# Kernel optimization log

Measured on AMD Instinct MI355X. Metric: run time of the kernel, lower is better.

The kernel has to match this reference:

```python
import jax, jax.numpy as jnp
import numpy as np
from jax import lax

SAMPLE_RATE = 44100.0  # config['std_sample_rate']
LOG9 = float(np.log(9.0))


def _drc_single(x, p):
    # param sanitization (apply_drc): NaN -> 0, 0 -> 1e-10, then rescale
    p = jnp.where(jnp.isnan(p), jnp.zeros_like(p), p)
    p = jnp.where(p == 0, jnp.full_like(p, 1e-10), p)
    threshold = -p[0] * 60.0
    ratio = p[1] * 10.0
    attack_time = jnp.maximum(p[2] / 10.0, 1e-4)
    release_time = jnp.maximum(p[3] * 3.0, 0.005)
    knee_dB = p[4] * 24.0
    makeup_gain_dB = p[5] * 20.0

    alpha_A = jnp.exp(-LOG9 / (SAMPLE_RATE * attack_time))
    alpha_R = jnp.exp(-LOG9 / (SAMPLE_RATE * release_time))

    # level detection in dB
    x_G = jnp.clip(20.0 * jnp.log10(jnp.abs(x) + 1e-8), -96.0, None)

    # static gain curve with soft knee (exactly as in source)
    below = 2.0 * (x_G - threshold) < -knee_dB
    above = 2.0 * (x_G - threshold) > knee_dB
    y_knee = x_G + (1.0 / ratio) * ((x_G - threshold + knee_dB) / 2.0) ** 2 / (2.0 * knee_dB)
    y_above = threshold + (x_G - threshold) / ratio
    y_G = jnp.where(below, x_G, jnp.where(above, y_above, y_knee))

    x_L = x_G - y_G  # gain reduction target (dB)

    # branching attack/release one-pole smoother; y_L[0] = 0, loop from n=1
    def step(y_prev, xl):
        alpha = jnp.where(xl > y_prev, alpha_A, alpha_R)
        y = alpha * y_prev + (1.0 - alpha) * xl
        return y, y

    _, y_tail = lax.scan(step, jnp.zeros((), x.dtype), x_L[1:])
    y_L = jnp.concatenate([jnp.zeros((1,), x.dtype), y_tail])
    y_L = jnp.clip(y_L, -96.0, None)

    y = x * jnp.power(10.0, -y_L / 20.0) * jnp.power(10.0, makeup_gain_dB / 20.0)
    # non-finite scrub (apply_drc tail)
    return jnp.where(jnp.isfinite(y), y, jnp.zeros_like(y))


def setup_inputs() -> dict:
    key = jax.random.key(0)
    kx, kp = jax.random.split(key)
    B, N = 16, 524288
    x = jax.random.normal(kx, (B, N), dtype=jnp.float32) * 0.3
    params = jax.random.uniform(kp, (B, 6), dtype=jnp.float32)
    return {"x": x, "params": params}


def reference(x, params):
    return jax.vmap(_drc_single)(x, params)
```

## Files before the change

### kernel.cpp

```cpp
#include <hip/hip_runtime.h>
#include <math.h>


#define SRATE 44100.0f
#define KSTEP 255
#define INTC  256
#define TILE2 32
#define NEG_INF -1e38f

static __device__ __forceinline__ float san(float p){
    p = isnan(p) ? 0.0f : p;
    p = (p == 0.0f) ? 1e-10f : p;
    return p;
}

struct Consts {
    float thr, invr, knee, i2k;
    float aA, aR, kAs, kRs, s;
    float mk;
    float LA, LR;
};

static __device__ __forceinline__ Consts get_consts(const float* __restrict__ P, int b){
    float p0 = san(P[b*6+0]);
    float p1 = san(P[b*6+1]);
    float p2 = san(P[b*6+2]);
    float p3 = san(P[b*6+3]);
    float p4 = san(P[b*6+4]);
    float p5 = san(P[b*6+5]);
    Consts c;
    c.thr  = -p0 * 60.0f;
    float ratio = p1 * 10.0f;
    c.invr = 1.0f / ratio;
    float atk = fmaxf(p2 / 10.0f, 1e-4f);
    float rel = fmaxf(p3 * 3.0f, 0.005f);
    c.knee = p4 * 24.0f;
    c.i2k  = 1.0f / (2.0f * c.knee);
    const float LOG9 = 2.1972245773362196f;
    const float INVLN2 = 1.4426950408889634f;
    c.aA = expf(-LOG9 / (SRATE * atk));
    c.aR = expf(-LOG9 / (SRATE * rel));
    c.LA = (-LOG9 / (SRATE * atk)) * INVLN2;
    c.LR = (-LOG9 / (SRATE * rel)) * INVLN2;
    c.s  = (c.aA <= c.aR) ? 1.0f : -1.0f;
    c.kAs = c.s * (1.0f - c.aA);
    c.kRs = c.s * (1.0f - c.aR);
    c.mk = exp2f((p5 * 20.0f) * 0.16609640474436813f);
    return c;
}

static __device__ __forceinline__ float compute_xl(float xin, const Consts& c){
    float ax = fabsf(xin) + 1e-8f;
    float xg = fmaxf(20.0f * log10f(ax), -96.0f);
    float d  = xg - c.thr;
    float t2 = d + d;
    float u  = (d + c.knee) * 0.5f;
    float yk = xg + (c.invr * (u * u)) * c.i2k;
    float ya = c.thr + d * c.invr;
    float yg = (t2 < -c.knee) ? xg : ((t2 > c.knee) ? ya : yk);
    return xg - yg;
}

template<int CTRL>
static __device__ __forceinline__ float maxdpp(float v){
    int t = __builtin_amdgcn_update_dpp(__float_as_int(v), __float_as_int(v),
                                        CTRL, 0xF, 0xF, false);
    return fmaxf(v, __int_as_float(t));
}

static __device__ __forceinline__ float rdlane(float v, int l){
    return __int_as_float(__builtin_amdgcn_readlane(__float_as_int(v), l));
}

#define STEPA(xli) { \
    float ca = c.kAs * (xli); \
    float cr = c.kRs * (xli); \
    float p3 = __shfl_up(M3, 1, 64); \
    p3 = (lane == 0) ? NEG_INF : p3; \
    M3 = fmaxf(fmaf(c.aA, M2, ca), fmaf(c.aR, M3, cr)); \
    M2 = fmaxf(fmaf(c.aA, M1, ca), fmaf(c.aR, M2, cr)); \
    M1 = fmaxf(fmaf(c.aA, M0, ca), fmaf(c.aR, M1, cr)); \
    M0 = fmaxf(fmaf(c.aA, p3, ca), fmaf(c.aR, M0, cr)); \
}

__global__ __launch_bounds__(256) void drc_passA(
    const float* __restrict__ x, const float* __restrict__ P,
    float* __restrict__ Mout, float* __restrict__ Movf,
    int N, int NBLK, int tailSteps, unsigned CAP4)
{
    const int lane = threadIdx.x & 63;
    const int gw = blockIdx.x * 4 + (threadIdx.x >> 6);
    const int batch = blockIdx.y;
    if (gw >= NBLK) return;
    Consts c = get_consts(P, batch);
    const int t = (gw == NBLK - 1) ? tailSteps : KSTEP;
    const size_t base = (size_t)batch * N;
    const int n0 = 2 + KSTEP * gw;

    const int i0 = n0 + 4 * lane;
    float xl0 = compute_xl(x[base + min(i0 + 0, N - 1)], c);
    float xl1 = compute_xl(x[base + min(i0 + 1, N - 1)], c);
    float xl2 = compute_xl(x[base + min(i0 + 2, N - 1)], c);
    float xl3 = compute_xl(x[base + min(i0 + 3, N - 1)], c);

    float M0 = (lane == 0) ? 0.0f : NEG_INF;
    float M1 = NEG_INF, M2 = NEG_INF, M3 = NEG_INF;

    if (t == KSTEP){
        for (int g = 0; g < 64; ++g){
            float xa0 = rdlane(xl0, g);
            float xa1 = rdlane(xl1, g);
            float xa2 = rdlane(xl2, g);
            float xa3 = rdlane(xl3, g);
            STEPA(xa0);
            STEPA(xa1);
            STEPA(xa2);
            if (g < 63) { STEPA(xa3); }
        }
    } else {
        for (int g = 0; g < 64; ++g){
            int ib = 4 * g;
            if (ib >= t) break;
            float xa0 = rdlane(xl0, g);
            float xa1 = rdlane(xl1, g);
            float xa2 = rdlane(xl2, g);
            float xa3 = rdlane(xl3, g);
            if (ib + 0 < t) { STEPA(xa0); }
            if (ib + 1 < t) { STEPA(xa1); }
            if (ib + 2 < t) { STEPA(xa2); }
            if (ib + 3 < t) { STEPA(xa3); }
        }
    }

    const size_t f4 = ((size_t)batch * NBLK + gw) * 64 + lane;
    float4 v = { M0, M1, M2, M3 };
    if (f4 < CAP4) ((float4*)Mout)[f4] = v;
    else           ((float4*)Movf)[f4 - CAP4] = v;
}

__global__ __launch_bounds__(192) void drc_chain(
    const float* __restrict__ x, const float* __restrict__ P,
    const float* __restrict__ Mout, const float* __restrict__ Movf,
    float* __restrict__ entries, int N, int NBLK, unsigned CAP4)
{
    const int batch = blockIdx.x;
    const int tid = threadIdx.x;
    const int lane = tid & 63;
    const int w = tid >> 6;
    Consts c = get_consts(P, batch);

    __shared__ float sM[2][TILE2 * INTC];

    const float4* outM4 = (const float4*)Mout;
    const float4* ovf4  = (const float4*)Movf;
    float* ent = entries + (size_t)batch * NBLK;

    const float j0 = (float)(4 * lane);
    float sl0 = exp2f((j0 + 0.0f) * c.LA + (float)(KSTEP - 4*lane - 0) * c.LR);
    float sl1 = exp2f((j0 + 1.0f) * c.LA + (float)(KSTEP - 4*lane - 1) * c.LR);
    float sl2 = exp2f((j0 + 2.0f) * c.LA + (float)(KSTEP - 4*lane - 2) * c.LR);
    float sl3 = exp2f((j0 + 3.0f) * c.LA + (float)(KSTEP - 4*lane - 3) * c.LR);

    float xl1 = compute_xl(x[(size_t)batch * N + 1], c);
    float z = fmaxf(c.kAs * xl1, c.kRs * xl1);

    const int NMAIN = NBLK - 1;
    const int ntiles = (NMAIN + TILE2 - 1) / TILE2;

    auto loadM4 = [&](size_t f4) -> float4 {
        return (f4 < CAP4) ? outM4[f4] : ovf4[f4 - CAP4];
    };

    auto stage = [&](int tile, int buf){
        const int s = tid - 64;
        const int b0 = tile * TILE2;
        const int cnt = min(TILE2, NMAIN - b0);
        const int total4 = cnt * 64;
        const size_t fb = ((size_t)batch * NBLK + b0) * 64;
        float4* dst = (float4*)&sM[buf][0];
        if (total4 == TILE2 * 64){
            float4 tmp[16];
            #pragma unroll
            for (int k = 0; k < 16; ++k) tmp[k] = loadM4(fb + (size_t)k * 128 + s);
            #pragma unroll
            for (int k = 0; k < 16; ++k) dst[k * 128 + s] = tmp[k];
        } else {
            for (int q = s; q < total4; q += 128) dst[q] = loadM4(fb + q);
        }
    };

    if (w > 0 && ntiles > 0) stage(0, 0);
    __syncthreads();

    float eacc = 0.0f;
    int ebase = 0;

    for (int tile = 0; tile < ntiles; ++tile){
        const int buf = tile & 1;
        if (w > 0){
            if (tile + 1 < ntiles) stage(tile + 1, buf ^ 1);
        } else {
            const int b0 = tile * TILE2;
            const int cnt = min(TILE2, NMAIN - b0);
            const float4* sb4 = (const float4*)&sM[buf][0];
            float4 m0 = sb4[lane];
            float4 m1 = sb4[min(1, cnt - 1) * 64 + lane];
            float4 m2 = sb4[min(2, cnt - 1) * 64 + lane];
            for (int it = 0; it < cnt; ++it){
                const int b = b0 + it;
                float4 mn = sb4[min(it + 3, cnt - 1) * 64 + lane];
                if (lane == (b & 63)) eacc = z;
                float f0 = fmaf(sl0, z, m0.x);
                float f1 = fmaf(sl1, z, m0.y);
                float f2 = fmaf(sl2, z, m0.z);
                float f3 = fmaf(sl3, z, m0.w);
                float tv = fmaxf(fmaxf(f0, f1), fmaxf(f2, f3));
                tv = maxdpp<0xB1>(tv);
                tv = maxdpp<0x4E>(tv);
                tv = maxdpp<0x141>(tv);
                tv = maxdpp<0x140>(tv);
                tv = maxdpp<0x142>(tv);
                tv = maxdpp<0x143>(tv);
                z = rdlane(tv, 63);
                if ((b & 63) == 63){ ent[ebase + lane] = eacc; ebase += 64; }
                m0 = m1; m1 = m2; m2 = mn;
            }
        }
        __syncthreads();
    }

    if (w == 0){
        const int bT = NBLK - 1;
        if (lane == (bT & 63)) eacc = z;
        const int rem = NBLK - ebase;
        if (lane < rem) ent[ebase + lane] = eacc;
    }
}

__global__ __launch_bounds__(256) void drc_pass3(
    const float* __restrict__ x, const float* __restrict__ P,
    const float* __restrict__ entries, float* __restrict__ out,
    int N, int NBLK, int tailSteps, int B)
{
    const int gid = blockIdx.x * blockDim.x + threadIdx.x;
    const int batch = gid / NBLK;
    if (batch >= B) return;
    const int b = gid - batch * NBLK;
    Consts c = get_consts(P, batch);
    const float KL = 0.16609640474436813f;
    const size_t base = (size_t)batch * N;

    float z = entries[(size_t)batch * NBLK + b];
    if (b == 0){
        float x0 = x[base + 0];
        float y0 = x0 * c.mk;
        out[base + 0] = isfinite(y0) ? y0 : 0.0f;
        float x1 = x[base + 1];
        float yl1 = fmaxf(c.s * z, -96.0f);
        float y1 = x1 * (exp2f(-yl1 * KL) * c.mk);
        out[base + 1] = isfinite(y1) ? y1 : 0.0f;
    }
    const int t = (b == NBLK - 1) ? tailSteps : KSTEP;
    const int n0 = 2 + b * KSTEP;

    #define P3STEP(xv) { \
        float xl = compute_xl(xv, c); \
        z = fmaxf(fmaf(c.aA, z, c.kAs * xl), fmaf(c.aR, z, c.kRs * xl)); }
    #define P3OUT(xv, dst) { \
        float yl = fmaxf(c.s * z, -96.0f); \
        float y = (xv) * (exp2f(-yl * KL) * c.mk); \
        dst = isfinite(y) ? y : 0.0f; }

    int i = 0;
    for (; i + 4 <= t; i += 4){
        const size_t n = base + n0 + i;
        float a0 = x[n + 0];
        float a1 = x[n + 1];
        float a2 = x[n + 2];
        float a3 = x[n + 3];
        float o0, o1, o2, o3;
        P3STEP(a0); P3OUT(a0, o0);
        P3STEP(a1); P3OUT(a1, o1);
        P3STEP(a2); P3OUT(a2, o2);
        P3STEP(a3); P3OUT(a3, o3);
        out[n + 0] = o0; out[n + 1] = o1; out[n + 2] = o2; out[n + 3] = o3;
    }
    for (; i < t; ++i){
        const size_t n = base + n0 + i;
        float a = x[n];
        float o;
        P3STEP(a); P3OUT(a, o);
        out[n] = o;
    }
}

extern "C" void kernel_launch(void* const* d_in, const int* in_sizes, int n_in,
                              void* d_out, int out_size, void* d_ws, size_t ws_size,
                              hipStream_t stream){
    const float* x = (const float*)d_in[0];
    const float* P = (const float*)d_in[1];
    float* out = (float*)d_out;
    float* ws  = (float*)d_ws;

    const int B = in_sizes[1] / 6;
    const int N = in_sizes[0] / B;

    const int NBLK = (N - 2 + KSTEP - 1) / KSTEP;
    const int tailSteps = (N - 2) - (NBLK - 1) * KSTEP;

    const unsigned OUT_CAP = (unsigned)out_size;
    const unsigned CAP4 = OUT_CAP / 4;

    float* entries = ws;
    size_t entN = (((size_t)B * NBLK) + 3) & ~(size_t)3;
    float* Movf = ws + entN;

    {
        dim3 g((NBLK + 3) / 4, B);
        drc_passA<<<g, 256, 0, stream>>>(x, P, out, Movf, N, NBLK, tailSteps, CAP4);
    }
    drc_chain<<<B, 192, 0, stream>>>(x, P, out, Movf, entries, N, NBLK, CAP4);
    {
        int total = B * NBLK;
        drc_pass3<<<(total + 255) / 256, 256, 0, stream>>>(x, P, entries, out,
                                                           N, NBLK, tailSteps, B);
    }
}
```

Before: 584.5 us.

## Shorten serial max-plus chain with 16-lane replicated reduction and swizzled LDS

The serial chain wave now gives each lane 16 slope terms instead of 4. Each 16-lane row therefore computes the full 256-wide max on its own, which cuts the cross-lane reduction to four DPP steps and removes the readlane broadcast from the critical path. The staged LDS tile is written with an XOR swizzle so the new strided float4 reads from the four row-replicas avoid bank conflicts. The loop is also unrolled three ways with rotating prefetch registers. The cost is more FMA and max work per step and higher register use in the latency-bound chain wave.

```diff
diff --git a/kernel.cpp b/kernel.cpp
--- a/kernel.cpp
+++ b/kernel.cpp
@@ -138,6 +138,33 @@
     else           ((float4*)Movf)[f4 - CAP4] = v;
 }
 
+#define SLP(e) exp2f((float)(16*rl+(e)) * c.LA + (float)(KSTEP-16*rl-(e)) * c.LR)
+
+#define BODY(M0v,M1v,M2v,M3v,bb) { \
+    const int b_ = (bb); \
+    if (lane == (b_ & 63)) eacc = z; \
+    float l0=fmaf(s0,z,M0v.x), l1=fmaf(s1,z,M0v.y), l2=fmaf(s2,z,M0v.z), l3=fmaf(s3,z,M0v.w); \
+    float l4=fmaf(s4,z,M1v.x), l5=fmaf(s5,z,M1v.y), l6=fmaf(s6,z,M1v.z), l7=fmaf(s7,z,M1v.w); \
+    float l8=fmaf(s8,z,M2v.x), l9=fmaf(s9,z,M2v.y), l10=fmaf(s10,z,M2v.z), l11=fmaf(s11,z,M2v.w); \
+    float l12=fmaf(s12,z,M3v.x), l13=fmaf(s13,z,M3v.y), l14=fmaf(s14,z,M3v.z), l15=fmaf(s15,z,M3v.w); \
+    float u0=fmaxf(fmaxf(l0,l1),fmaxf(l2,l3)); \
+    float u1=fmaxf(fmaxf(l4,l5),fmaxf(l6,l7)); \
+    float u2=fmaxf(fmaxf(l8,l9),fmaxf(l10,l11)); \
+    float u3=fmaxf(fmaxf(l12,l13),fmaxf(l14,l15)); \
+    float v_=fmaxf(fmaxf(u0,u1),fmaxf(u2,u3)); \
+    v_=maxdpp<0xB1>(v_); v_=maxdpp<0x4E>(v_); \
+    v_=maxdpp<0x141>(v_); v_=maxdpp<0x140>(v_); \
+    z=v_; \
+    if ((b_ & 63) == 63){ ent[ebase+lane]=eacc; ebase+=64; } \
+}
+
+#define LD(d0,d1,d2,d3, idx) { \
+    const float4* sb4_ = (const float4*)sb; \
+    int ii_ = (idx) * 64; \
+    d0 = sb4_[ii_ + q0s]; d1 = sb4_[ii_ + q1s]; \
+    d2 = sb4_[ii_ + q2s]; d3 = sb4_[ii_ + q3s]; \
+}
+
 __global__ __launch_bounds__(192) void drc_chain(
     const float* __restrict__ x, const float* __restrict__ P,
     const float* __restrict__ Mout, const float* __restrict__ Movf,
@@ -146,6 +173,7 @@
     const int batch = blockIdx.x;
     const int tid = threadIdx.x;
     const int lane = tid & 63;
+    const int rl = lane & 15;
     const int w = tid >> 6;
     Consts c = get_consts(P, batch);
 
@@ -155,14 +183,18 @@
     const float4* ovf4  = (const float4*)Movf;
     float* ent = entries + (size_t)batch * NBLK;
 
-    const float j0 = (float)(4 * lane);
-    float sl0 = exp2f((j0 + 0.0f) * c.LA + (float)(KSTEP - 4*lane - 0) * c.LR);
-    float sl1 = exp2f((j0 + 1.0f) * c.LA + (float)(KSTEP - 4*lane - 1) * c.LR);
-    float sl2 = exp2f((j0 + 2.0f) * c.LA + (float)(KSTEP - 4*lane - 2) * c.LR);
-    float sl3 = exp2f((j0 + 3.0f) * c.LA + (float)(KSTEP - 4*lane - 3) * c.LR);
-
-    float xl1 = compute_xl(x[(size_t)batch * N + 1], c);
-    float z = fmaxf(c.kAs * xl1, c.kRs * xl1);
+    const int q0s = (4*rl + 0) ^ (rl & 7);
+    const int q1s = (4*rl + 1) ^ (rl & 7);
+    const int q2s = (4*rl + 2) ^ (rl & 7);
+    const int q3s = (4*rl + 3) ^ (rl & 7);
+
+    float s0=SLP(0), s1=SLP(1), s2=SLP(2), s3=SLP(3);
+    float s4=SLP(4), s5=SLP(5), s6=SLP(6), s7=SLP(7);
+    float s8=SLP(8), s9=SLP(9), s10=SLP(10), s11=SLP(11);
+    float s12=SLP(12), s13=SLP(13), s14=SLP(14), s15=SLP(15);
+
+    float xl1v = compute_xl(x[(size_t)batch * N + 1], c);
+    float z = fmaxf(c.kAs * xl1v, c.kRs * xl1v);
 
     const int NMAIN = NBLK - 1;
     const int ntiles = (NMAIN + TILE2 - 1) / TILE2;
@@ -172,7 +204,7 @@
     };
 
     auto stage = [&](int tile, int buf){
-        const int s = tid - 64;
+        const int sI = tid - 64;
         const int b0 = tile * TILE2;
         const int cnt = min(TILE2, NMAIN - b0);
         const int total4 = cnt * 64;
@@ -181,11 +213,20 @@
         if (total4 == TILE2 * 64){
             float4 tmp[16];
             #pragma unroll
-            for (int k = 0; k < 16; ++k) tmp[k] = loadM4(fb + (size_t)k * 128 + s);
+            for (int k = 0; k < 16; ++k) tmp[k] = loadM4(fb + (size_t)k * 128 + sI);
             #pragma unroll
-            for (int k = 0; k < 16; ++k) dst[k * 128 + s] = tmp[k];
+            for (int k = 0; k < 16; ++k){
+                int q  = k * 128 + sI;
+                int lq = q & 63;
+                int qs = (q & ~63) | (lq ^ ((lq >> 2) & 7));
+                dst[qs] = tmp[k];
+            }
         } else {
-            for (int q = s; q < total4; q += 128) dst[q] = loadM4(fb + q);
+            for (int q = sI; q < total4; q += 128){
+                int lq = q & 63;
+                int qs = (q & ~63) | (lq ^ ((lq >> 2) & 7));
+                dst[qs] = loadM4(fb + q);
+            }
         }
     };
 
@@ -202,29 +243,23 @@
         } else {
             const int b0 = tile * TILE2;
             const int cnt = min(TILE2, NMAIN - b0);
-            const float4* sb4 = (const float4*)&sM[buf][0];
-            float4 m0 = sb4[lane];
-            float4 m1 = sb4[min(1, cnt - 1) * 64 + lane];
-            float4 m2 = sb4[min(2, cnt - 1) * 64 + lane];
-            for (int it = 0; it < cnt; ++it){
-                const int b = b0 + it;
-                float4 mn = sb4[min(it + 3, cnt - 1) * 64 + lane];
-                if (lane == (b & 63)) eacc = z;
-                float f0 = fmaf(sl0, z, m0.x);
-                float f1 = fmaf(sl1, z, m0.y);
-                float f2 = fmaf(sl2, z, m0.z);
-                float f3 = fmaf(sl3, z, m0.w);
-                float tv = fmaxf(fmaxf(f0, f1), fmaxf(f2, f3));
-                tv = maxdpp<0xB1>(tv);
-                tv = maxdpp<0x4E>(tv);
-                tv = maxdpp<0x141>(tv);
-                tv = maxdpp<0x140>(tv);
-                tv = maxdpp<0x142>(tv);
-                tv = maxdpp<0x143>(tv);
-                z = rdlane(tv, 63);
-                if ((b & 63) == 63){ ent[ebase + lane] = eacc; ebase += 64; }
-                m0 = m1; m1 = m2; m2 = mn;
+            const float* sb = &sM[buf][0];
+            float4 A0,A1,A2,A3, B0,B1,B2,B3, C0,C1,C2,C3;
+            LD(A0,A1,A2,A3, 0)
+            LD(B0,B1,B2,B3, min(1, cnt - 1))
+            LD(C0,C1,C2,C3, min(2, cnt - 1))
+            int it = 0;
+            for (; it + 3 <= cnt; it += 3){
+                BODY(A0,A1,A2,A3, b0 + it)
+                LD(A0,A1,A2,A3, min(it + 3, cnt - 1))
+                BODY(B0,B1,B2,B3, b0 + it + 1)
+                LD(B0,B1,B2,B3, min(it + 4, cnt - 1))
+                BODY(C0,C1,C2,C3, b0 + it + 2)
+                LD(C0,C1,C2,C3, min(it + 5, cnt - 1))
             }
+            if (it     < cnt){ BODY(A0,A1,A2,A3, b0 + it)     }
+            if (it + 1 < cnt){ BODY(B0,B1,B2,B3, b0 + it + 1) }
+            if (it + 2 < cnt){ BODY(C0,C1,C2,C3, b0 + it + 2) }
         }
         __syncthreads();
     }
```

Result: slower. 601.1 us (+2.8%).
